# Performance work log

Hardware: AMD Instinct MI355X
Metric: run time of the kernel (lower is better)

## Reference

```python
import jax, jax.numpy as jnp
import numpy as np

# --- static config (matches init_kwargs) ---
DIM_Z, DIM_A, DIM_U, K, GRU_H, DIM_OBS = 32, 16, 4, 8, 64, 16
BATCH, TLEN = 128, 256
Q_STD, R_STD, QR_REG, TEMP = 0.05, 0.05, 1e-3, 1.0


def setup_inputs() -> dict:
    key = jax.random.key(0)
    ks = jax.random.split(key, 10)
    a_seq = jax.random.normal(ks[0], (BATCH, TLEN, DIM_A), jnp.float32)
    h_obs = jax.random.normal(ks[1], (BATCH, DIM_OBS), jnp.float32)
    # scale dynamics so the T-step recursion is stable (spectral radius < 1)
    A_matrices = jax.random.normal(ks[2], (K, DIM_Z, DIM_Z), jnp.float32) * (0.6 / np.sqrt(DIM_Z))
    C_matrices = jax.random.normal(ks[3], (K, DIM_A, DIM_Z), jnp.float32) * (1.0 / np.sqrt(DIM_Z))
    B_matrices = jax.random.normal(ks[4], (K, DIM_Z, DIM_U), jnp.float32) * 0.1
    u_seq = jax.random.normal(ks[5], (BATCH, TLEN, DIM_U), jnp.float32)
    mask = jnp.ones((BATCH, TLEN), jnp.float32)
    # learned params: P_0 = 5*I, cholesky of Q_std*I / R_std*I
    P_0 = 5.0 * jnp.eye(DIM_Z, dtype=jnp.float32)
    mat_Q = np.sqrt(Q_STD).astype(np.float32) * jnp.eye(DIM_Z, dtype=jnp.float32)
    mat_R = np.sqrt(R_STD).astype(np.float32) * jnp.eye(DIM_A, dtype=jnp.float32)
    # alpha network: GRU cell over concat(a_prev, h_obs, z_prev, a_next_all) + linear head
    d_in = DIM_A + DIM_OBS + DIM_Z + K * DIM_A
    gru_Wx = jax.random.normal(ks[6], (d_in, 3 * GRU_H), jnp.float32) / np.sqrt(d_in)
    gru_Wh = jax.random.normal(ks[7], (GRU_H, 3 * GRU_H), jnp.float32) / np.sqrt(GRU_H)
    gru_b = jnp.zeros((3 * GRU_H,), jnp.float32)
    out_W = jax.random.normal(ks[8], (GRU_H, K), jnp.float32) / np.sqrt(GRU_H)
    out_b = jnp.zeros((K,), jnp.float32)
    return dict(a_seq=a_seq, h_obs=h_obs, A_matrices=A_matrices, C_matrices=C_matrices,
                B_matrices=B_matrices, u_seq=u_seq, mask=mask, P_0=P_0, mat_Q=mat_Q,
                mat_R=mat_R, gru_Wx=gru_Wx, gru_Wh=gru_Wh, gru_b=gru_b,
                out_W=out_W, out_b=out_b, epoch=100)


def _mT(M):
    return jnp.swapaxes(M, -1, -2)


def _kf_forward(a_seq, h_obs, A_matrices, C_matrices, B_matrices, u_seq, mask,
                P_0, mat_Q, mat_R, gru_Wx, gru_Wh, gru_b, out_W, out_b):
    Bn, Tn, da = a_seq.shape
    dz = A_matrices.shape[-1]
    I_z = jnp.eye(dz, dtype=a_seq.dtype)
    I_a = jnp.eye(da, dtype=a_seq.dtype)
    Q = mat_Q @ mat_Q.T + QR_REG * I_z
    R = mat_R @ mat_R.T + QR_REG * I_a
    sg = jax.lax.stop_gradient

    def gru_cell(x, h):
        gx = x @ gru_Wx + gru_b
        gh = h @ gru_Wh
        xr, xz, xn = jnp.split(gx, 3, axis=-1)
        hr, hz, hn = jnp.split(gh, 3, axis=-1)
        r = jax.nn.sigmoid(xr + hr)
        zg = jax.nn.sigmoid(xz + hz)
        n = jnp.tanh(xn + r * hn)
        return (1.0 - zg) * n + zg * h

    def step(carry, xs):
        z_prev, P, gh, C_prev = carry
        a_k, u_k, m_k = xs          # [B,da], [B,du], [B]
        mk = m_k[:, None]           # [B,1]
        # per-expert one-step predictions (IMM likelihoods)
        zj = jnp.einsum('kij,bj->bki', A_matrices, z_prev)        # [B,K,dz]
        aj = jnp.einsum('kai,bki->bka', C_matrices, zj)           # [B,K,da]
        a_next_all = aj.reshape(Bn, K * da)
        log_lik = -jnp.sum((a_k[:, None, :] - aj) ** 2, axis=-1)  # [B,K]
        alpha_imm = jax.nn.softmax(log_lik, axis=-1) * mk
        # alpha network (inputs detached as in original)
        a_prev = sg(jnp.einsum('bai,bi->ba', C_prev, z_prev))
        x_in = jnp.concatenate([a_prev, h_obs, sg(z_prev), a_next_all], axis=-1)
        gh = gru_cell(x_in, gh)
        alpha = jax.nn.softmax((gh @ out_W + out_b) / TEMP, axis=-1)  # [B,K]
        # mixture matrices
        A_k = jnp.einsum('bk,kij->bij', alpha, A_matrices)
        C_k = jnp.einsum('bk,kai->bai', alpha, C_matrices)
        # predict / innovate
        z = jnp.einsum('bij,bj->bi', A_k, z_prev)
        a_hat = jnp.einsum('bai,bi->ba', C_k, z)
        r_k = a_k - a_hat
        S = C_k @ P @ _mT(C_k) + R + 1e-4 * I_a
        Kg = _mT(jnp.linalg.solve(_mT(S), C_k @ _mT(P)))          # [B,dz,da]
        Kg = Kg * mk[:, :, None]
        IKC = I_z - Kg @ C_k
        P_f = IKC @ P @ _mT(IKC) + Kg @ R @ _mT(Kg)
        P_f = 0.5 * (P_f + _mT(P_f)) + 1e-3 * I_z
        z_loc = z + jnp.einsum('bia,ba->bi', Kg, r_k)
        tril = jnp.linalg.cholesky(P_f)
        z_filt = z_loc  # eval mode: mean of MVN(z_loc, P_f)
        # epoch >= 20 -> p_true = 0 -> always kalman reconstruction
        a_filt = jnp.einsum('bai,bi->ba', C_k, z_filt)
        z_pred = jnp.einsum('bij,bj->bi', A_k, z_filt)  # eval: no Q-noise
        B_k = jnp.einsum('bk,kiu->biu', alpha, B_matrices)
        z_pred = z_pred + jnp.einsum('biu,bu->bi', B_k, u_k)
        P_p = A_k @ P_f @ _mT(A_k) + Q
        P_p = 0.5 * (P_p + _mT(P_p)) + 1e-3 * I_z
        a_pred = jnp.einsum('bai,bi->ba', C_k, z_pred)
        new_carry = (z_filt, P_p, gh, sg(C_k))
        ys = (z_filt, P_f, z_loc, tril, z_pred, P_p, a_filt, a_pred, S, alpha, alpha_imm)
        return new_carry, ys

    z0 = jnp.zeros((Bn, dz), a_seq.dtype)
    P_init = jnp.broadcast_to(P_0, (Bn, dz, dz))
    gh0 = jnp.zeros((Bn, GRU_H), a_seq.dtype)
    C0 = jnp.broadcast_to(C_matrices[0], (Bn, da, dz))
    xs = (jnp.swapaxes(a_seq, 0, 1), jnp.swapaxes(u_seq, 0, 1), mask.T)
    _, ys = jax.lax.scan(step, (z0, P_init, gh0, C0), xs)
    outs = jax.tree.map(lambda y: jnp.swapaxes(y, 0, 1), ys)  # [T,B,...] -> [B,T,...]
    return outs + (R, Q)


def reference(a_seq, h_obs, A_matrices, C_matrices, B_matrices, u_seq, mask,
              P_0, mat_Q, mat_R, gru_Wx, gru_Wh, gru_b, out_W, out_b, epoch):
    # epoch=100 semantics baked in: temp=1, p_true=0, no burn-in detach, eval mode
    return _kf_forward(a_seq, h_obs, A_matrices, C_matrices, B_matrices, u_seq, mask,
                       P_0, mat_Q, mat_R, gru_Wx, gru_Wh, gru_b, out_W, out_b)
```

## Files before the change

### kernel.cpp

```cpp
#include <hip/hip_runtime.h>
#include <math.h>

#define NT 256
#define FMA4(acc,u,bv) {acc.x+=(u)*(bv).x; acc.y+=(u)*(bv).y; acc.z+=(u)*(bv).z; acc.w+=(u)*(bv).w;}

__device__ __forceinline__ float sigf(float x){ return 1.0f/(1.0f+expf(-x)); }
__device__ __forceinline__ float rdlane(float v, int l){
  return __int_as_float(__builtin_amdgcn_readlane(__float_as_int(v), l));
}
__device__ __forceinline__ float dot4(float4 a, float4 b){
  return a.x*b.x + a.y*b.y + a.z*b.z + a.w*b.w;
}

__launch_bounds__(NT, 1)
__global__ void kf_fwd(const float* __restrict__ a_seq, const float* __restrict__ h_obs,
  const float* __restrict__ Amat, const float* __restrict__ Cmat, const float* __restrict__ Bmat,
  const float* __restrict__ u_seq, const float* __restrict__ mask, const float* __restrict__ P0,
  const float* __restrict__ matQ, const float* __restrict__ matR,
  const float* __restrict__ Wx, const float* __restrict__ Wh, const float* __restrict__ gbias,
  const float* __restrict__ outW, const float* __restrict__ outb, float* __restrict__ out)
{
  constexpr int T=256, B=128;
  constexpr int L6=36, L0=20;
  constexpr size_t BT=(size_t)B*T;
  const size_t off_zf=0;
  const size_t off_Pf=off_zf+BT*32;
  const size_t off_zl=off_Pf+BT*1024;
  const size_t off_tr=off_zl+BT*32;
  const size_t off_zp=off_tr+BT*1024;
  const size_t off_Pp=off_zp+BT*32;
  const size_t off_af=off_Pp+BT*1024;
  const size_t off_ap=off_af+BT*16;
  const size_t off_S =off_ap+BT*16;
  const size_t off_al=off_S +BT*256;
  const size_t off_ai=off_al+BT*8;
  const size_t off_R =off_ai+BT*8;
  const size_t off_Q =off_R +256;

  __shared__ __align__(16) float sA[8*32*L6];
  __shared__ __align__(16) float sC[8*16*L6];
  __shared__ __align__(16) float W12[48*192];
  __shared__ __align__(16) float gxh[192];
  __shared__ __align__(16) float sBm[1024];
  __shared__ __align__(16) float souWT[512];
  __shared__ __align__(16) float soutb8[8];
  __shared__ __align__(16) float P[32*L6], T1m[32*L6], T3m[32*L6], Qm[32*L6];
  __shared__ __align__(16) float Ak2[2][32*L6], AkT2[2][32*L6];
  __shared__ __align__(16) float Ck[16*L6], CPm[16*L6];
  __shared__ __align__(16) float CPT[32*L0], Kg[32*L0];
  __shared__ __align__(16) float Sm[16*L0], Rm[16*L0], Sinv[16*L0];
  __shared__ __align__(16) float Linv[16*17];
  __shared__ __align__(16) float Bk[128];
  __shared__ __align__(16) float zj[256], aj[128];
  __shared__ __align__(16) float gx[192], ghl[192];
  __shared__ __align__(16) float zc[32], znew[32], zloc[32], zpred[32], ghs[64];
  __shared__ __align__(16) float aprevv[16], hob[16];
  __shared__ __align__(16) float ak[16], uk[4], rk[16], alpha8[8];
  __shared__ __align__(16) float ys[16], ws[16];
  __shared__ float mvs2[2];

  const int tid  = threadIdx.x;
  const int wid  = tid>>6;
  const int lane = tid&63;
  const int b = blockIdx.x;

  for (int e=tid; e<8192; e+=NT){ int k=e>>10, i=(e>>5)&31, j=e&31; sA[(k*32+i)*L6+j]=Amat[e]; }
  for (int e=tid; e<4096; e+=NT){ int k=e>>9, a=(e>>5)&15, i=e&31; sC[(k*16+a)*L6+i]=Cmat[e]; }
  for (int e=tid; e<1024; e+=NT) sBm[e]=Bmat[e];
  for (int e=tid; e<512; e+=NT){ int r=e>>6, q=e&63; souWT[r*64+q]=outW[q*8+r]; }
  if (tid<8) soutb8[tid]=outb[tid];
  for (int e=tid; e<1024; e+=NT){
    int i=e>>5, j=e&31;
    float s=0.f;
    #pragma unroll 8
    for (int k=0;k<32;k++) s += matQ[i*32+k]*matQ[j*32+k];
    Qm[i*L6+j]=s+(i==j?0.001f:0.f);
    P[i*L6+j]=P0[e];
  }
  for (int e=tid; e<256; e+=NT){
    int i=e>>4, j=e&15;
    float s=0.f;
    #pragma unroll
    for (int k=0;k<16;k++) s += matR[i*16+k]*matR[j*16+k];
    Rm[i*L0+j]=s+(i==j?0.001f:0.f);
  }
  for (int e=tid; e<16*L6; e+=NT) Ck[e]=0.f;
  if (tid<32) zc[tid]=0.f;
  if (tid<64) ghs[tid]=0.f;
  for (int e=tid; e<192; e+=NT) ghl[e]=0.f;
  if (tid<16) hob[tid]=h_obs[b*16+tid];
  __syncthreads();

  if (tid<48){
    const int c0=tid*4;
    #pragma unroll
    for (int a=0;a<16;a++)
      *(float4*)&W12[(32+a)*192+c0] = *(const float4*)(Wx+(size_t)a*192+c0);
    float4 acc=*(const float4*)(gbias+c0);
    #pragma unroll
    for (int i=0;i<16;i++){
      float4 w=*(const float4*)(Wx+(size_t)(16+i)*192+c0);
      float hv=hob[i];
      FMA4(acc,hv,w);
    }
    *(float4*)&gxh[c0]=acc;
  }
  for (int ic=0; ic<4; ++ic){
    float4 Mi[8];
    if (tid<48){
// ... 30 lines not shown
      #pragma unroll
      for (int ii=0;ii<8;ii++)
        *(float4*)&W12[(ic*8+ii)*192+c0]=Mi[ii];
    }
  }
  if (b==0){
    for (int e=tid;e<256;e+=NT) out[off_R+e]=Rm[(e>>4)*L0+(e&15)];
    for (int e=tid;e<1024;e+=NT) out[off_Q+e]=Qm[(e>>5)*L6+(e&31)];
  }
  __syncthreads();

  for (int t=0;t<T;t++){
    const size_t bt=(size_t)b*T+t;
    const int pc=t&1, pp=pc^1;

    if (wid==0){
      if (lane==0) mvs2[pc]=mask[bt];
      float4 zq[8];
      #pragma unroll
      for (int q=0;q<8;q++) zq[q]=*(const float4*)&zc[q*4];
      if (lane<16){
        float s=0.f;
        #pragma unroll
        for (int q=0;q<8;q++) s+=dot4(*(const float4*)&Ck[lane*L6+q*4], zq[q]);
        aprevv[lane]=s;
      }
      if (lane<48){
        const int c0=lane*4;
        float4 A0=*(const float4*)&gxh[c0];
        float4 A1=make_float4(0.f,0.f,0.f,0.f), A2=A1, A3=A1;
        #pragma unroll
        for (int q=0;q<8;q++){
          float4 zv=zq[q];
          float4 w0=*(const float4*)&W12[(q*4+0)*192+c0];
          float4 w1=*(const float4*)&W12[(q*4+1)*192+c0];
          float4 w2=*(const float4*)&W12[(q*4+2)*192+c0];
          float4 w3=*(const float4*)&W12[(q*4+3)*192+c0];
          FMA4(A0,zv.x,w0); FMA4(A1,zv.y,w1); FMA4(A2,zv.z,w2); FMA4(A3,zv.w,w3);
        }
        #pragma unroll
        for (int q=0;q<4;q++){
          float4 av=*(const float4*)&aprevv[q*4];
          float4 w0=*(const float4*)&W12[(32+q*4+0)*192+c0];
          float4 w1=*(const float4*)&W12[(32+q*4+1)*192+c0];
          float4 w2=*(const float4*)&W12[(32+q*4+2)*192+c0];
          float4 w3=*(const float4*)&W12[(32+q*4+3)*192+c0];
          FMA4(A0,av.x,w0); FMA4(A1,av.y,w1); FMA4(A2,av.z,w2); FMA4(A3,av.w,w3);
// ... 5 lines not shown
      {
        float r =sigf(gx[lane]+ghl[lane]);
        float zg=sigf(gx[64+lane]+ghl[64+lane]);
        float n =tanhf(gx[128+lane]+r*ghl[128+lane]);
        float h=ghs[lane];
        ghs[lane]=(1.f-zg)*n+zg*h;
      }
      if (lane<8){
        float s=soutb8[lane];
        #pragma unroll
        for (int q=0;q<16;q++){
          float4 g=*(const float4*)&ghs[q*4];
          float4 w=*(const float4*)&souWT[lane*64+q*4];
          s+=dot4(g,w);
        }
        float m8=s;
        m8=fmaxf(m8,__shfl_xor(m8,1)); m8=fmaxf(m8,__shfl_xor(m8,2)); m8=fmaxf(m8,__shfl_xor(m8,4));
        float e2=expf(s-m8);
        float ss=e2;
        ss+=__shfl_xor(ss,1); ss+=__shfl_xor(ss,2); ss+=__shfl_xor(ss,4);
        float av=e2/ss;
        alpha8[lane]=av;
        out[off_al+bt*8+lane]=av;
      }
    } else if (wid==1){
      if (t>0){
        const size_t bt1=bt-1;
        #pragma unroll
        for (int q=0;q<4;q++){
          int e=lane+64*q; int a2=e>>4, b2=e&15;
          float s=0.f;
          #pragma unroll
          for (int k=0;k<16;k++) s+=Linv[k*17+a2]*Linv[k*17+b2];
          Sinv[a2*L0+b2]=s;
        }
        {
          int i0=lane>>2, aq=lane&3;
          float4 k0=make_float4(0.f,0.f,0.f,0.f), k1=k0;
          #pragma unroll
          for (int q=0;q<4;q++){
            float4 ca=*(const float4*)&CPT[i0*L0+q*4];
            float4 cb=*(const float4*)&CPT[(i0+16)*L0+q*4];
            float4 v0=*(const float4*)&Sinv[(q*4+0)*L0+aq*4];
            float4 v1=*(const float4*)&Sinv[(q*4+1)*L0+aq*4];
            float4 v2=*(const float4*)&Sinv[(q*4+2)*L0+aq*4];
            float4 v3=*(const float4*)&Sinv[(q*4+3)*L0+aq*4];
// ... 25 lines not shown
            FMA4(q0,-a0.y,bv); FMA4(q1,-a1.y,bv); FMA4(q2,-a2.y,bv); FMA4(q3,-a3.y,bv);
            bv=*(const float4*)&CPm[(q*4+2)*L6+j0];
            FMA4(q0,-a0.z,bv); FMA4(q1,-a1.z,bv); FMA4(q2,-a2.z,bv); FMA4(q3,-a3.z,bv);
            bv=*(const float4*)&CPm[(q*4+3)*L6+j0];
            FMA4(q0,-a0.w,bv); FMA4(q1,-a1.w,bv); FMA4(q2,-a2.w,bv); FMA4(q3,-a3.w,bv);
          }
          int d0=i0-j0;
          if (d0>=0&&d0<4){ if(d0==0)q0.x+=1e-3f; else if(d0==1)q0.y+=1e-3f; else if(d0==2)q0.z+=1e-3f; else q0.w+=1e-3f; }
          int d1=i0+1-j0;
          if (d1>=0&&d1<4){ if(d1==0)q1.x+=1e-3f; else if(d1==1)q1.y+=1e-3f; else if(d1==2)q1.z+=1e-3f; else q1.w+=1e-3f; }
          int d2=i0+2-j0;
          if (d2>=0&&d2<4){ if(d2==0)q2.x+=1e-3f; else if(d2==1)q2.y+=1e-3f; else if(d2==2)q2.z+=1e-3f; else q2.w+=1e-3f; }
          int d3=i0+3-j0;
          if (d3>=0&&d3<4){ if(d3==0)q3.x+=1e-3f; else if(d3==1)q3.y+=1e-3f; else if(d3==2)q3.z+=1e-3f; else q3.w+=1e-3f; }
          *(float4*)&T3m[(i0+0)*L6+j0]=q0;
          *(float4*)&T3m[(i0+1)*L6+j0]=q1;
          *(float4*)&T3m[(i0+2)*L6+j0]=q2;
          *(float4*)&T3m[(i0+3)*L6+j0]=q3;
          *(float4*)&out[off_Pf+bt1*1024+(i0+0)*32+j0]=q0;
          *(float4*)&out[off_Pf+bt1*1024+(i0+1)*32+j0]=q1;
          *(float4*)&out[off_Pf+bt1*1024+(i0+2)*32+j0]=q2;
          *(float4*)&out[off_Pf+bt1*1024+(i0+3)*32+j0]=q3;
        }
      }
    } else if (wid==2){
      if (t>0){
        const size_t bt1=bt-1;
        float4 zq[8];
        #pragma unroll
        for (int q=0;q<8;q++) zq[q]=*(const float4*)&zc[q*4];
        if (lane<32){
          float s=0.f;
          #pragma unroll
          for (int q=0;q<8;q++) s+=dot4(*(const float4*)&Ak2[pp][lane*L6+q*4], zq[q]);
          float4 bk=*(const float4*)&Bk[lane*4];
          float4 u4=*(const float4*)&uk[0];
          s+=dot4(bk,u4);
          zpred[lane]=s;
          out[off_zp+bt1*32+lane]=s;
        }
        if (lane>=32 && lane<48){
          int a=lane-32;
          float s=0.f;
          #pragma unroll
          for (int q=0;q<8;q++) s+=dot4(*(const float4*)&Ck[a*L6+q*4], zq[q]);
          out[off_af+bt1*16+a]=s;
        }
        if (lane<16){
          float s=0.f;
          #pragma unroll
          for (int q=0;q<8;q++)
            s+=dot4(*(const float4*)&Ck[lane*L6+q*4], *(const float4*)&zpred[q*4]);
          out[off_ap+bt1*16+lane]=s;
        }
      }
    } else {
      if (lane<16) ak[lane]=a_seq[bt*16+lane];
      float mv=mask[bt];
      float4 zq[8];
      #pragma unroll
      for (int q=0;q<8;q++) zq[q]=*(const float4*)&zc[q*4];
      #pragma unroll
      for (int r=0;r<4;r++){
        int e=lane+64*r; int k=e>>5, i=e&31;
        float s=0.f;
        #pragma unroll
        for (int q=0;q<8;q++) s+=dot4(*(const float4*)&sA[(k*32+i)*L6+q*4], zq[q]);
        zj[e]=s;
      }
      #pragma unroll
      for (int r=0;r<2;r++){
        int e=lane+64*r; int k=e>>4, a=e&15;
        float s=0.f;
        #pragma unroll
        for (int q=0;q<8;q++) s+=dot4(*(const float4*)&sC[(k*16+a)*L6+q*4], *(const float4*)&zj[k*32+q*4]);
        aj[e]=s;
      }
      if (lane<8){
        float s=0.f;
        #pragma unroll
        for (int q=0;q<4;q++){
          float4 av=*(const float4*)&ak[q*4];
          float4 jv=*(const float4*)&aj[lane*16+q*4];
          float dx=av.x-jv.x, dy=av.y-jv.y, dz=av.z-jv.z, dw=av.w-jv.w;
          s+=dx*dx+dy*dy+dz*dz+dw*dw;
        }
        float llv=-s;
        float m8=llv;
        m8=fmaxf(m8,__shfl_xor(m8,1)); m8=fmaxf(m8,__shfl_xor(m8,2)); m8=fmaxf(m8,__shfl_xor(m8,4));
        float e2=expf(llv-m8);
        float ss=e2;
        ss+=__shfl_xor(ss,1); ss+=__shfl_xor(ss,2); ss+=__shfl_xor(ss,4);
        out[off_ai+bt*8+lane]=e2/ss*mv;
      }
    }
    __syncthreads();

    if (wid==0 || wid==3){
      float alr[8];
      float4 a0v=*(const float4*)&alpha8[0], a1v=*(const float4*)&alpha8[4];
      alr[0]=a0v.x; alr[1]=a0v.y; alr[2]=a0v.z; alr[3]=a0v.w;
      alr[4]=a1v.x; alr[5]=a1v.y; alr[6]=a1v.z; alr[7]=a1v.w;
      if (wid==0){
        #pragma unroll
        for (int r=0;r<2;r++){
          int e=lane+64*r; int i=e>>3, qd=e&7;
          float4 acc=make_float4(0.f,0.f,0.f,0.f);
          #pragma unroll
          for (int k=0;k<8;k++){
            float4 av=*(const float4*)&sA[(k*32+i)*L6+qd*4];
            FMA4(acc,alr[k],av);
          }
          *(float4*)&Ak2[pc][i*L6+qd*4]=acc;
          AkT2[pc][(qd*4+0)*L6+i]=acc.x; AkT2[pc][(qd*4+1)*L6+i]=acc.y;
          AkT2[pc][(qd*4+2)*L6+i]=acc.z; AkT2[pc][(qd*4+3)*L6+i]=acc.w;
        }
        #pragma unroll
        for (int r=0;r<2;r++){
          int e=lane+64*r;
          float s=0.f;
          #pragma unroll
          for (int k=0;k<8;k++) s+=alr[k]*sBm[k*128+e];
          Bk[e]=s;
        }
        if (lane<32){
          float s=0.f;
          #pragma unroll
          for (int k=0;k<8;k++) s+=alr[k]*zj[k*32+lane];
          znew[lane]=s;
        }
      } else {
        #pragma unroll
        for (int r=2;r<4;r++){
          int e=lane+64*r; int i=e>>3, qd=e&7;
          float4 acc=make_float4(0.f,0.f,0.f,0.f);
          #pragma unroll
          for (int k=0;k<8;k++){
            float4 av=*(const float4*)&sA[(k*32+i)*L6+qd*4];
            FMA4(acc,alr[k],av);
          }
          *(float4*)&Ak2[pc][i*L6+qd*4]=acc;
          AkT2[pc][(qd*4+0)*L6+i]=acc.x; AkT2[pc][(qd*4+1)*L6+i]=acc.y;
          AkT2[pc][(qd*4+2)*L6+i]=acc.z; AkT2[pc][(qd*4+3)*L6+i]=acc.w;
        }
        #pragma unroll
        for (int r=0;r<2;r++){
          int e=lane+64*r; int a=e>>3, qd=e&7;
          float4 acc=make_float4(0.f,0.f,0.f,0.f);
          #pragma unroll
          for (int k=0;k<8;k++){
            float4 cv=*(const float4*)&sC[(k*16+a)*L6+qd*4];
            FMA4(acc,alr[k],cv);
          }
          *(float4*)&Ck[a*L6+qd*4]=acc;
        }
      }
    } else if (wid==1){
      if (t>0){
        const size_t bt1=bt-1;
        int row=lane<32?lane:31;
        float trl[32];
        #pragma unroll
        for (int q=0;q<8;q++){
          float4 v=*(const float4*)&T3m[row*L6+q*4];
          trl[q*4+0]=v.x; trl[q*4+1]=v.y; trl[q*4+2]=v.z; trl[q*4+3]=v.w;
        }
        #pragma unroll
        for (int c=0;c<32;c++){
          float d=rdlane(trl[c],c);
          float inv=rsqrtf(d);
          float lc=(lane==c)?d*inv:trl[c]*inv;
          trl[c]=lc;
          #pragma unroll
          for (int j=c+1;j<32;j++) trl[j]-=lc*rdlane(lc,j);
        }
        if (lane<32){
          #pragma unroll
          for (int q=0;q<8;q++){
            float t0=(q*4+0<=lane)?trl[q*4+0]:0.f;
            float t1=(q*4+1<=lane)?trl[q*4+1]:0.f;
            float t2=(q*4+2<=lane)?trl[q*4+2]:0.f;
            float t3=(q*4+3<=lane)?trl[q*4+3]:0.f;
            *(float4*)&out[off_tr+bt1*1024+lane*32+q*4]=make_float4(t0,t1,t2,t3);
          }
        }
      }
    } else {
      if (t>0){
        const size_t bt1=bt-1;
        {
          const int i0=(lane>>3)*4, j0=(lane&7)*4;
          float4 q0=make_float4(0.f,0.f,0.f,0.f), q1=q0, q2=q0, q3=q0;
          #pragma unroll 4
          for (int q=0;q<8;q++){
            float4 a0=*(const float4*)&Ak2[pp][(i0+0)*L6+q*4];
            float4 a1=*(const float4*)&Ak2[pp][(i0+1)*L6+q*4];
            float4 a2=*(const float4*)&Ak2[pp][(i0+2)*L6+q*4];
            float4 a3=*(const float4*)&Ak2[pp][(i0+3)*L6+q*4];
            float4 bv;
            bv=*(const float4*)&T3m[(q*4+0)*L6+j0];
            FMA4(q0,a0.x,bv); FMA4(q1,a1.x,bv); FMA4(q2,a2.x,bv); FMA4(q3,a3.x,bv);
            bv=*(const float4*)&T3m[(q*4+1)*L6+j0];
            FMA4(q0,a0.y,bv); FMA4(q1,a1.y,bv); FMA4(q2,a2.y,bv); FMA4(q3,a3.y,bv);
            bv=*(const float4*)&T3m[(q*4+2)*L6+j0];
            FMA4(q0,a0.z,bv); FMA4(q1,a1.z,bv); FMA4(q2,a2.z,bv); FMA4(q3,a3.z,bv);
            bv=*(const float4*)&T3m[(q*4+3)*L6+j0];
            FMA4(q0,a0.w,bv); FMA4(q1,a1.w,bv); FMA4(q2,a2.w,bv); FMA4(q3,a3.w,bv);
          }
          *(float4*)&T1m[(i0+0)*L6+j0]=q0;
          *(float4*)&T1m[(i0+1)*L6+j0]=q1;
          *(float4*)&T1m[(i0+2)*L6+j0]=q2;
          *(float4*)&T1m[(i0+3)*L6+j0]=q3;
// ... 18 lines not shown
            float4 a1=*(const float4*)&T1m[(i0+1)*L6+q*4];
            float4 a2=*(const float4*)&T1m[(i0+2)*L6+q*4];
            float4 a3=*(const float4*)&T1m[(i0+3)*L6+q*4];
            float4 bv;
            bv=*(const float4*)&AkT2[pp][(q*4+0)*L6+j0];
            FMA4(q0,a0.x,bv); FMA4(q1,a1.x,bv); FMA4(q2,a2.x,bv); FMA4(q3,a3.x,bv);
            bv=*(const float4*)&AkT2[pp][(q*4+1)*L6+j0];
            FMA4(q0,a0.y,bv); FMA4(q1,a1.y,bv); FMA4(q2,a2.y,bv); FMA4(q3,a3.y,bv);
            bv=*(const float4*)&AkT2[pp][(q*4+2)*L6+j0];
            FMA4(q0,a0.z,bv); FMA4(q1,a1.z,bv); FMA4(q2,a2.z,bv); FMA4(q3,a3.z,bv);
            bv=*(const float4*)&AkT2[pp][(q*4+3)*L6+j0];
            FMA4(q0,a0.w,bv); FMA4(q1,a1.w,bv); FMA4(q2,a2.w,bv); FMA4(q3,a3.w,bv);
          }
          *(float4*)&P[(i0+0)*L6+j0]=q0;
          *(float4*)&P[(i0+1)*L6+j0]=q1;
          *(float4*)&P[(i0+2)*L6+j0]=q2;
          *(float4*)&P[(i0+3)*L6+j0]=q3;
          *(float4*)&out[off_Pp+bt1*1024+(i0+0)*32+j0]=q0;
          *(float4*)&out[off_Pp+bt1*1024+(i0+1)*32+j0]=q1;
          *(float4*)&out[off_Pp+bt1*1024+(i0+2)*32+j0]=q2;
          *(float4*)&out[off_Pp+bt1*1024+(i0+3)*32+j0]=q3;
        }
      }
    }
    __syncthreads();

    if (wid==0){
      {
        int qd=lane&7, a0=lane>>3;
        float4 d0=make_float4(0.f,0.f,0.f,0.f), d1=d0;
        #pragma unroll 2
        for (int q=0;q<8;q++){
          float4 c0=*(const float4*)&Ck[a0*L6+q*4];
          float4 c1=*(const float4*)&Ck[(a0+8)*L6+q*4];
          float4 p0=*(const float4*)&P[(q*4+0)*L6+qd*4];
          float4 p1=*(const float4*)&P[(q*4+1)*L6+qd*4];
          float4 p2=*(const float4*)&P[(q*4+2)*L6+qd*4];
          float4 p3=*(const float4*)&P[(q*4+3)*L6+qd*4];
          FMA4(d0,c0.x,p0); FMA4(d0,c0.y,p1); FMA4(d0,c0.z,p2); FMA4(d0,c0.w,p3);
          FMA4(d1,c1.x,p0); FMA4(d1,c1.y,p1); FMA4(d1,c1.z,p2); FMA4(d1,c1.w,p3);
        }
        *(float4*)&CPm[a0*L6+qd*4]=d0;
        *(float4*)&CPm[(a0+8)*L6+qd*4]=d1;
        CPT[(qd*4+0)*L0+a0]=d0.x; CPT[(qd*4+1)*L0+a0]=d0.y;
        CPT[(qd*4+2)*L0+a0]=d0.z; CPT[(qd*4+3)*L0+a0]=d0.w;
        CPT[(qd*4+0)*L0+a0+8]=d1.x; CPT[(qd*4+1)*L0+a0+8]=d1.y;
        CPT[(qd*4+2)*L0+a0+8]=d1.z; CPT[(qd*4+3)*L0+a0+8]=d1.w;
      }
      if (lane<16){
        float s=0.f;
        #pragma unroll
        for (int q=0;q<8;q++) s+=dot4(*(const float4*)&Ck[lane*L6+q*4], *(const float4*)&znew[q*4]);
        rk[lane]=ak[lane]-s;
      }
      {
        int a2=lane>>2, cq=lane&3;
        float s0=0.f,s1=0.f,s2=0.f,s3=0.f;
        #pragma unroll 2
        for (int q=0;q<8;q++){
          float4 cp=*(const float4*)&CPm[a2*L6+q*4];
          s0+=dot4(cp,*(const float4*)&Ck[(cq*4+0)*L6+q*4]);
          s1+=dot4(cp,*(const float4*)&Ck[(cq*4+1)*L6+q*4]);
          s2+=dot4(cp,*(const float4*)&Ck[(cq*4+2)*L6+q*4]);
          s3+=dot4(cp,*(const float4*)&Ck[(cq*4+3)*L6+q*4]);
        }
        float4 rm=*(const float4*)&Rm[a2*L0+cq*4];
        s0+=rm.x+((a2==cq*4+0)?1e-4f:0.f);
        s1+=rm.y+((a2==cq*4+1)?1e-4f:0.f);
        s2+=rm.z+((a2==cq*4+2)?1e-4f:0.f);
        s3+=rm.w+((a2==cq*4+3)?1e-4f:0.f);
        float4 sv=make_float4(s0,s1,s2,s3);
        *(float4*)&Sm[a2*L0+cq*4]=sv;
        *(float4*)&out[off_S+bt*256+lane*4]=sv;
      }
      {
        int row=lane<16?lane:15;
        float Sr[16], invd[16];
        #pragma unroll
        for (int q=0;q<4;q++){
          float4 v=*(const float4*)&Sm[row*L0+q*4];
          Sr[q*4+0]=v.x; Sr[q*4+1]=v.y; Sr[q*4+2]=v.z; Sr[q*4+3]=v.w;
        }
        #pragma unroll
        for (int c=0;c<16;c++){
          float d=rdlane(Sr[c],c);
          float inv=rsqrtf(d);
          invd[c]=inv;
// ... 37 lines not shown
          s+=dot4(*(const float4*)&CPT[lane*L0+q*4], *(const float4*)&ws[q*4]);
        zloc[lane]=s;
        zc[lane]=s;
        out[off_zf+bt*32+lane]=s;
        out[off_zl+bt*32+lane]=s;
      }
    } else if (wid==1){
      if (lane<48){
        const int c0=lane*4;
        float4 A0=make_float4(0.f,0.f,0.f,0.f), A1=A0, A2=A0, A3=A0;
        #pragma unroll
        for (int q=0;q<16;q++){
          float4 gv=*(const float4*)&ghs[q*4];
          float4 w0=*(const float4*)(Wh+(size_t)(q*4+0)*192+c0);
          float4 w1=*(const float4*)(Wh+(size_t)(q*4+1)*192+c0);
          float4 w2=*(const float4*)(Wh+(size_t)(q*4+2)*192+c0);
          float4 w3=*(const float4*)(Wh+(size_t)(q*4+3)*192+c0);
          FMA4(A0,gv.x,w0); FMA4(A1,gv.y,w1); FMA4(A2,gv.z,w2); FMA4(A3,gv.w,w3);
        }
        float4 g=make_float4(A0.x+A1.x+A2.x+A3.x, A0.y+A1.y+A2.y+A3.y,
                             A0.z+A1.z+A2.z+A3.z, A0.w+A1.w+A2.w+A3.w);
        *(float4*)&ghl[c0]=g;
      }
    } else if (wid==2){
      if (lane<4) uk[lane]=u_seq[bt*4+lane];
    }
    __syncthreads();
  }

  {
    const size_t btL=(size_t)b*T+(T-1);
    const int pl=(T-1)&1;
    if (wid==1){
      #pragma unroll
      for (int q=0;q<4;q++){
        int e=lane+64*q; int a2=e>>4, b2=e&15;
        float s=0.f;
        #pragma unroll
        for (int k=0;k<16;k++) s+=Linv[k*17+a2]*Linv[k*17+b2];
        Sinv[a2*L0+b2]=s;
      }
      {
        int i0=lane>>2, aq=lane&3;
        float4 k0=make_float4(0.f,0.f,0.f,0.f), k1=k0;
        #pragma unroll
        for (int q=0;q<4;q++){
          float4 ca=*(const float4*)&CPT[i0*L0+q*4];
          float4 cb=*(const float4*)&CPT[(i0+16)*L0+q*4];
// ... 29 lines not shown
          FMA4(q0,-a0.y,bv); FMA4(q1,-a1.y,bv); FMA4(q2,-a2.y,bv); FMA4(q3,-a3.y,bv);
          bv=*(const float4*)&CPm[(q*4+2)*L6+j0];
          FMA4(q0,-a0.z,bv); FMA4(q1,-a1.z,bv); FMA4(q2,-a2.z,bv); FMA4(q3,-a3.z,bv);
          bv=*(const float4*)&CPm[(q*4+3)*L6+j0];
          FMA4(q0,-a0.w,bv); FMA4(q1,-a1.w,bv); FMA4(q2,-a2.w,bv); FMA4(q3,-a3.w,bv);
        }
        int d0=i0-j0;
        if (d0>=0&&d0<4){ if(d0==0)q0.x+=1e-3f; else if(d0==1)q0.y+=1e-3f; else if(d0==2)q0.z+=1e-3f; else q0.w+=1e-3f; }
        int d1=i0+1-j0;
        if (d1>=0&&d1<4){ if(d1==0)q1.x+=1e-3f; else if(d1==1)q1.y+=1e-3f; else if(d1==2)q1.z+=1e-3f; else q1.w+=1e-3f; }
        int d2=i0+2-j0;
        if (d2>=0&&d2<4){ if(d2==0)q2.x+=1e-3f; else if(d2==1)q2.y+=1e-3f; else if(d2==2)q2.z+=1e-3f; else q2.w+=1e-3f; }
        int d3=i0+3-j0;
        if (d3>=0&&d3<4){ if(d3==0)q3.x+=1e-3f; else if(d3==1)q3.y+=1e-3f; else if(d3==2)q3.z+=1e-3f; else q3.w+=1e-3f; }
        *(float4*)&T3m[(i0+0)*L6+j0]=q0;
        *(float4*)&T3m[(i0+1)*L6+j0]=q1;
        *(float4*)&T3m[(i0+2)*L6+j0]=q2;
        *(float4*)&T3m[(i0+3)*L6+j0]=q3;
        *(float4*)&out[off_Pf+btL*1024+(i0+0)*32+j0]=q0;
        *(float4*)&out[off_Pf+btL*1024+(i0+1)*32+j0]=q1;
        *(float4*)&out[off_Pf+btL*1024+(i0+2)*32+j0]=q2;
        *(float4*)&out[off_Pf+btL*1024+(i0+3)*32+j0]=q3;
      }
    } else if (wid==2){
      float4 zq[8];
      #pragma unroll
      for (int q=0;q<8;q++) zq[q]=*(const float4*)&zc[q*4];
      if (lane<32){
        float s=0.f;
        #pragma unroll
        for (int q=0;q<8;q++) s+=dot4(*(const float4*)&Ak2[pl][lane*L6+q*4], zq[q]);
        float4 bk=*(const float4*)&Bk[lane*4];
        float4 u4=*(const float4*)&uk[0];
        s+=dot4(bk,u4);
        zpred[lane]=s;
        out[off_zp+btL*32+lane]=s;
      }
      if (lane>=32 && lane<48){
        int a=lane-32;
        float s=0.f;
        #pragma unroll
        for (int q=0;q<8;q++) s+=dot4(*(const float4*)&Ck[a*L6+q*4], zq[q]);
        out[off_af+btL*16+a]=s;
      }
      if (lane<16){
        float s=0.f;
        #pragma unroll
        for (int q=0;q<8;q++)
          s+=dot4(*(const float4*)&Ck[lane*L6+q*4], *(const float4*)&zpred[q*4]);
        out[off_ap+btL*16+lane]=s;
      }
    }
    __syncthreads();
    if (wid==1){
      int row=lane<32?lane:31;
      float trl[32];
      #pragma unroll
      for (int q=0;q<8;q++){
        float4 v=*(const float4*)&T3m[row*L6+q*4];
        trl[q*4+0]=v.x; trl[q*4+1]=v.y; trl[q*4+2]=v.z; trl[q*4+3]=v.w;
      }
      #pragma unroll
      for (int c=0;c<32;c++){
        float d=rdlane(trl[c],c);
        float inv=rsqrtf(d);
        float lc=(lane==c)?d*inv:trl[c]*inv;
        trl[c]=lc;
        #pragma unroll
        for (int j=c+1;j<32;j++) trl[j]-=lc*rdlane(lc,j);
      }
      if (lane<32){
        #pragma unroll
        for (int q=0;q<8;q++){
          float t0=(q*4+0<=lane)?trl[q*4+0]:0.f;
          float t1=(q*4+1<=lane)?trl[q*4+1]:0.f;
          float t2=(q*4+2<=lane)?trl[q*4+2]:0.f;
          float t3=(q*4+3<=lane)?trl[q*4+3]:0.f;
          *(float4*)&out[off_tr+btL*1024+lane*32+q*4]=make_float4(t0,t1,t2,t3);
        }
      }
    } else if (wid==2){
      {
        const int i0=(lane>>3)*4, j0=(lane&7)*4;
        float4 q0=make_float4(0.f,0.f,0.f,0.f), q1=q0, q2=q0, q3=q0;
        #pragma unroll 4
        for (int q=0;q<8;q++){
          float4 a0=*(const float4*)&Ak2[pl][(i0+0)*L6+q*4];
          float4 a1=*(const float4*)&Ak2[pl][(i0+1)*L6+q*4];
          float4 a2=*(const float4*)&Ak2[pl][(i0+2)*L6+q*4];
          float4 a3=*(const float4*)&Ak2[pl][(i0+3)*L6+q*4];
          float4 bv;
          bv=*(const float4*)&T3m[(q*4+0)*L6+j0];
          FMA4(q0,a0.x,bv); FMA4(q1,a1.x,bv); FMA4(q2,a2.x,bv); FMA4(q3,a3.x,bv);
          bv=*(const float4*)&T3m[(q*4+1)*L6+j0];
          FMA4(q0,a0.y,bv); FMA4(q1,a1.y,bv); FMA4(q2,a2.y,bv); FMA4(q3,a3.y,bv);
          bv=*(const float4*)&T3m[(q*4+2)*L6+j0];
          FMA4(q0,a0.z,bv); FMA4(q1,a1.z,bv); FMA4(q2,a2.z,bv); FMA4(q3,a3.z,bv);
          bv=*(const float4*)&T3m[(q*4+3)*L6+j0];
          FMA4(q0,a0.w,bv); FMA4(q1,a1.w,bv); FMA4(q2,a2.w,bv); FMA4(q3,a3.w,bv);
        }
        *(float4*)&T1m[(i0+0)*L6+j0]=q0;
        *(float4*)&T1m[(i0+1)*L6+j0]=q1;
        *(float4*)&T1m[(i0+2)*L6+j0]=q2;
        *(float4*)&T1m[(i0+3)*L6+j0]=q3;
// ... 13 lines not shown
        int d3=i0+3-j0;
        if (d3>=0&&d3<4){ if(d3==0)q3.x+=1e-3f; else if(d3==1)q3.y+=1e-3f; else if(d3==2)q3.z+=1e-3f; else q3.w+=1e-3f; }
        #pragma unroll 4
        for (int q=0;q<8;q++){
          float4 a0=*(const float4*)&T1m[(i0+0)*L6+q*4];
          float4 a1=*(const float4*)&T1m[(i0+1)*L6+q*4];
          float4 a2=*(const float4*)&T1m[(i0+2)*L6+q*4];
          float4 a3=*(const float4*)&T1m[(i0+3)*L6+q*4];
          float4 bv;
          bv=*(const float4*)&AkT2[pl][(q*4+0)*L6+j0];
          FMA4(q0,a0.x,bv); FMA4(q1,a1.x,bv); FMA4(q2,a2.x,bv); FMA4(q3,a3.x,bv);
          bv=*(const float4*)&AkT2[pl][(q*4+1)*L6+j0];
          FMA4(q0,a0.y,bv); FMA4(q1,a1.y,bv); FMA4(q2,a2.y,bv); FMA4(q3,a3.y,bv);
          bv=*(const float4*)&AkT2[pl][(q*4+2)*L6+j0];
          FMA4(q0,a0.z,bv); FMA4(q1,a1.z,bv); FMA4(q2,a2.z,bv); FMA4(q3,a3.z,bv);
          bv=*(const float4*)&AkT2[pl][(q*4+3)*L6+j0];
          FMA4(q0,a0.w,bv); FMA4(q1,a1.w,bv); FMA4(q2,a2.w,bv); FMA4(q3,a3.w,bv);
        }
        *(float4*)&out[off_Pp+btL*1024+(i0+0)*32+j0]=q0;
        *(float4*)&out[off_Pp+btL*1024+(i0+1)*32+j0]=q1;
        *(float4*)&out[off_Pp+btL*1024+(i0+2)*32+j0]=q2;
        *(float4*)&out[off_Pp+btL*1024+(i0+3)*32+j0]=q3;
      }
    }
  }
}

extern "C" void kernel_launch(void* const* d_in, const int* in_sizes, int n_in,
                              void* d_out, int out_size, void* d_ws, size_t ws_size,
                              hipStream_t stream) {
  kf_fwd<<<128, NT, 0, stream>>>(
    (const float*)d_in[0],
    (const float*)d_in[1],
    (const float*)d_in[2],
    (const float*)d_in[3],
    (const float*)d_in[4],
    (const float*)d_in[5],
    (const float*)d_in[6],
    (const float*)d_in[7],
    (const float*)d_in[8],
    (const float*)d_in[9],
    (const float*)d_in[10],
    (const float*)d_in[11],
    (const float*)d_in[12],
    (const float*)d_in[13],
    (const float*)d_in[14],
// ... 3 lines not shown
```

Baseline: 2.626 ms.

## Reschedule per-step warp work to remove a barrier phase per timestep

Warp 0 now builds the mixed C matrix immediately after the softmax, into a double-buffered Ck2. Each step's work is redistributed across the four warps: the Cholesky factorisation moves to warp 2, the mixed A/B construction moves to warp 3, and the P-prediction matmul moves to warp 1. The intent is to drop one of the three __syncthreads phases per timestep and balance the critical path across warps. In exchange, the extra C buffer adds shared memory, and the warp handling the Cholesky and A mixing now carries a heavier serial load.

Measured after the change: 2.407 ms, median of 2. 1.09x faster.

```diff
diff --git a/kernel.cpp b/kernel.cpp
--- a/kernel.cpp
+++ b/kernel.cpp
@@ -46,7 +46,8 @@
   __shared__ __align__(16) float soutb8[8];
   __shared__ __align__(16) float P[32*L6], T1m[32*L6], T3m[32*L6], Qm[32*L6];
   __shared__ __align__(16) float Ak2[2][32*L6], AkT2[2][32*L6];
-  __shared__ __align__(16) float Ck[16*L6], CPm[16*L6];
+  __shared__ __align__(16) float Ck2[2][16*L6];
+  __shared__ __align__(16) float CPm[16*L6];
   __shared__ __align__(16) float CPT[32*L0], Kg[32*L0];
   __shared__ __align__(16) float Sm[16*L0], Rm[16*L0], Sinv[16*L0];
   __shared__ __align__(16) float Linv[16*17];
@@ -84,7 +85,7 @@
     for (int k=0;k<16;k++) s += matR[i*16+k]*matR[j*16+k];
     Rm[i*L0+j]=s+(i==j?0.001f:0.f);
   }
-  for (int e=tid; e<16*L6; e+=NT) Ck[e]=0.f;
+  for (int e=tid; e<16*L6; e+=NT){ Ck2[0][e]=0.f; Ck2[1][e]=0.f; }
   if (tid<32) zc[tid]=0.f;
   if (tid<64) ghs[tid]=0.f;
   for (int e=tid; e<192; e+=NT) ghl[e]=0.f;
@@ -161,7 +162,7 @@
       if (lane<16){
         float s=0.f;
         #pragma unroll
-        for (int q=0;q<8;q++) s+=dot4(*(const float4*)&Ck[lane*L6+q*4], zq[q]);
+        for (int q=0;q<8;q++) s+=dot4(*(const float4*)&Ck2[pp][lane*L6+q*4], zq[q]);
         aprevv[lane]=s;
       }
       if (lane<48){
@@ -213,6 +214,23 @@
         float av=e2/ss;
         alpha8[lane]=av;
         out[off_al+bt*8+lane]=av;
+      }
+      {
+        float alr[8];
+        float4 a0v=*(const float4*)&alpha8[0], a1v=*(const float4*)&alpha8[4];
+        alr[0]=a0v.x; alr[1]=a0v.y; alr[2]=a0v.z; alr[3]=a0v.w;
+        alr[4]=a1v.x; alr[5]=a1v.y; alr[6]=a1v.z; alr[7]=a1v.w;
+        #pragma unroll
+        for (int r=0;r<2;r++){
+          int e=lane+64*r; int a=e>>3, qd=e&7;
+          float4 acc=make_float4(0.f,0.f,0.f,0.f);
+          #pragma unroll
+          for (int k=0;k<8;k++){
+            float4 cv=*(const float4*)&sC[(k*16+a)*L6+qd*4];
+            FMA4(acc,alr[k],cv);
+          }
+          *(float4*)&Ck2[pc][a*L6+qd*4]=acc;
+        }
       }
     } else if (wid==1){
       if (t>0){
@@ -284,172 +302,6 @@
           *(float4*)&out[off_Pf+bt1*1024+(i0+2)*32+j0]=q2;
           *(float4*)&out[off_Pf+bt1*1024+(i0+3)*32+j0]=q3;
         }
-      }
-    } else if (wid==2){
-      if (t>0){
-        const size_t bt1=bt-1;
-        float4 zq[8];
-        #pragma unroll
-        for (int q=0;q<8;q++) zq[q]=*(const float4*)&zc[q*4];
-        if (lane<32){
-          float s=0.f;
-          #pragma unroll
-          for (int q=0;q<8;q++) s+=dot4(*(const float4*)&Ak2[pp][lane*L6+q*4], zq[q]);
-          float4 bk=*(const float4*)&Bk[lane*4];
-          float4 u4=*(const float4*)&uk[0];
-          s+=dot4(bk,u4);
-          zpred[lane]=s;
-          out[off_zp+bt1*32+lane]=s;
-        }
-        if (lane>=32 && lane<48){
-          int a=lane-32;
-          float s=0.f;
-          #pragma unroll
-          for (int q=0;q<8;q++) s+=dot4(*(const float4*)&Ck[a*L6+q*4], zq[q]);
-          out[off_af+bt1*16+a]=s;
-        }
-        if (lane<16){
-          float s=0.f;
-          #pragma unroll
-          for (int q=0;q<8;q++)
-            s+=dot4(*(const float4*)&Ck[lane*L6+q*4], *(const float4*)&zpred[q*4]);
-          out[off_ap+bt1*16+lane]=s;
-        }
-      }
-    } else {
-      if (lane<16) ak[lane]=a_seq[bt*16+lane];
-      float mv=mask[bt];
-      float4 zq[8];
-      #pragma unroll
-      for (int q=0;q<8;q++) zq[q]=*(const float4*)&zc[q*4];
-      #pragma unroll
-      for (int r=0;r<4;r++){
-        int e=lane+64*r; int k=e>>5, i=e&31;
-        float s=0.f;
-        #pragma unroll
-        for (int q=0;q<8;q++) s+=dot4(*(const float4*)&sA[(k*32+i)*L6+q*4], zq[q]);
-        zj[e]=s;
-      }
-      #pragma unroll
-      for (int r=0;r<2;r++){
-        int e=lane+64*r; int k=e>>4, a=e&15;
-        float s=0.f;
-        #pragma unroll
-        for (int q=0;q<8;q++) s+=dot4(*(const float4*)&sC[(k*16+a)*L6+q*4], *(const float4*)&zj[k*32+q*4]);
-        aj[e]=s;
-      }
-      if (lane<8){
-        float s=0.f;
-        #pragma unroll
-        for (int q=0;q<4;q++){
-          float4 av=*(const float4*)&ak[q*4];
-          float4 jv=*(const float4*)&aj[lane*16+q*4];
-          float dx=av.x-jv.x, dy=av.y-jv.y, dz=av.z-jv.z, dw=av.w-jv.w;
-          s+=dx*dx+dy*dy+dz*dz+dw*dw;
-        }
-        float llv=-s;
-        float m8=llv;
-        m8=fmaxf(m8,__shfl_xor(m8,1)); m8=fmaxf(m8,__shfl_xor(m8,2)); m8=fmaxf(m8,__shfl_xor(m8,4));
-        float e2=expf(llv-m8);
-        float ss=e2;
-        ss+=__shfl_xor(ss,1); ss+=__shfl_xor(ss,2); ss+=__shfl_xor(ss,4);
-        out[off_ai+bt*8+lane]=e2/ss*mv;
-      }
-    }
-    __syncthreads();
-
-    if (wid==0 || wid==3){
-      float alr[8];
-      float4 a0v=*(const float4*)&alpha8[0], a1v=*(const float4*)&alpha8[4];
-      alr[0]=a0v.x; alr[1]=a0v.y; alr[2]=a0v.z; alr[3]=a0v.w;
-      alr[4]=a1v.x; alr[5]=a1v.y; alr[6]=a1v.z; alr[7]=a1v.w;
-      if (wid==0){
-        #pragma unroll
-        for (int r=0;r<2;r++){
-          int e=lane+64*r; int i=e>>3, qd=e&7;
-          float4 acc=make_float4(0.f,0.f,0.f,0.f);
-          #pragma unroll
-          for (int k=0;k<8;k++){
-            float4 av=*(const float4*)&sA[(k*32+i)*L6+qd*4];
-            FMA4(acc,alr[k],av);
-          }
-          *(float4*)&Ak2[pc][i*L6+qd*4]=acc;
-          AkT2[pc][(qd*4+0)*L6+i]=acc.x; AkT2[pc][(qd*4+1)*L6+i]=acc.y;
-          AkT2[pc][(qd*4+2)*L6+i]=acc.z; AkT2[pc][(qd*4+3)*L6+i]=acc.w;
-        }
-        #pragma unroll
-        for (int r=0;r<2;r++){
-          int e=lane+64*r;
-          float s=0.f;
-          #pragma unroll
-          for (int k=0;k<8;k++) s+=alr[k]*sBm[k*128+e];
-          Bk[e]=s;
-        }
-        if (lane<32){
-          float s=0.f;
-          #pragma unroll
-          for (int k=0;k<8;k++) s+=alr[k]*zj[k*32+lane];
-          znew[lane]=s;
-        }
-      } else {
-        #pragma unroll
-        for (int r=2;r<4;r++){
-          int e=lane+64*r; int i=e>>3, qd=e&7;
-          float4 acc=make_float4(0.f,0.f,0.f,0.f);
-          #pragma unroll
-          for (int k=0;k<8;k++){
-            float4 av=*(const float4*)&sA[(k*32+i)*L6+qd*4];
-            FMA4(acc,alr[k],av);
-          }
-          *(float4*)&Ak2[pc][i*L6+qd*4]=acc;
-          AkT2[pc][(qd*4+0)*L6+i]=acc.x; AkT2[pc][(qd*4+1)*L6+i]=acc.y;
-          AkT2[pc][(qd*4+2)*L6+i]=acc.z; AkT2[pc][(qd*4+3)*L6+i]=acc.w;
-        }
-        #pragma unroll
-        for (int r=0;r<2;r++){
-          int e=lane+64*r; int a=e>>3, qd=e&7;
-          float4 acc=make_float4(0.f,0.f,0.f,0.f);
-          #pragma unroll
-          for (int k=0;k<8;k++){
-            float4 cv=*(const float4*)&sC[(k*16+a)*L6+qd*4];
-            FMA4(acc,alr[k],cv);
-          }
-          *(float4*)&Ck[a*L6+qd*4]=acc;
-        }
-      }
-    } else if (wid==1){
-      if (t>0){
-        const size_t bt1=bt-1;
-        int row=lane<32?lane:31;
-        float trl[32];
-        #pragma unroll
-        for (int q=0;q<8;q++){
-          float4 v=*(const float4*)&T3m[row*L6+q*4];
-          trl[q*4+0]=v.x; trl[q*4+1]=v.y; trl[q*4+2]=v.z; trl[q*4+3]=v.w;
-        }
-        #pragma unroll
-        for (int c=0;c<32;c++){
-          float d=rdlane(trl[c],c);
-          float inv=rsqrtf(d);
-          float lc=(lane==c)?d*inv:trl[c]*inv;
-          trl[c]=lc;
-          #pragma unroll
-          for (int j=c+1;j<32;j++) trl[j]-=lc*rdlane(lc,j);
-        }
-        if (lane<32){
-          #pragma unroll
-          for (int q=0;q<8;q++){
-            float t0=(q*4+0<=lane)?trl[q*4+0]:0.f;
-            float t1=(q*4+1<=lane)?trl[q*4+1]:0.f;
-            float t2=(q*4+2<=lane)?trl[q*4+2]:0.f;
-            float t3=(q*4+3<=lane)?trl[q*4+3]:0.f;
-            *(float4*)&out[off_tr+bt1*1024+lane*32+q*4]=make_float4(t0,t1,t2,t3);
-          }
-        }
-      }
-    } else {
-      if (t>0){
-        const size_t bt1=bt-1;
         {
           const int i0=(lane>>3)*4, j0=(lane&7)*4;
           float4 q0=make_float4(0.f,0.f,0.f,0.f), q1=q0, q2=q0, q3=q0;
@@ -514,17 +366,93 @@
           *(float4*)&out[off_Pp+bt1*1024+(i0+3)*32+j0]=q3;
         }
       }
+    } else if (wid==2){
+      if (t>0){
+        const size_t bt1=bt-1;
+        float4 zq[8];
+        #pragma unroll
+        for (int q=0;q<8;q++) zq[q]=*(const float4*)&zc[q*4];
+        if (lane<32){
+          float s=0.f;
+          #pragma unroll
+          for (int q=0;q<8;q++) s+=dot4(*(const float4*)&Ak2[pp][lane*L6+q*4], zq[q]);
+          float4 bk=*(const float4*)&Bk[lane*4];
+          float4 u4=*(const float4*)&uk[0];
+          s+=dot4(bk,u4);
+          zpred[lane]=s;
+          out[off_zp+bt1*32+lane]=s;
+        }
+        if (lane>=32 && lane<48){
+          int a=lane-32;
+          float s=0.f;
+          #pragma unroll
+          for (int q=0;q<8;q++) s+=dot4(*(const float4*)&Ck2[pp][a*L6+q*4], zq[q]);
+          out[off_af+bt1*16+a]=s;
+        }
+        if (lane<16){
+          float s=0.f;
+          #pragma unroll
+          for (int q=0;q<8;q++)
+            s+=dot4(*(const float4*)&Ck2[pp][lane*L6+q*4], *(const float4*)&zpred[q*4]);
+          out[off_ap+bt1*16+lane]=s;
+        }
+      }
+    } else {
+      if (lane<16) ak[lane]=a_seq[bt*16+lane];
+      float mv=mask[bt];
+      float4 zq[8];
+      #pragma unroll
+      for (int q=0;q<8;q++) zq[q]=*(const float4*)&zc[q*4];
+      #pragma unroll
+      for (int r=0;r<4;r++){
+        int e=lane+64*r; int k=e>>5, i=e&31;
+        float s=0.f;
+        #pragma unroll
+        for (int q=0;q<8;q++) s+=dot4(*(const float4*)&sA[(k*32+i)*L6+q*4], zq[q]);
+        zj[e]=s;
+      }
+      #pragma unroll
+      for (int r=0;r<2;r++){
+        int e=lane+64*r; int k=e>>4, a=e&15;
+        float s=0.f;
+        #pragma unroll
+        for (int q=0;q<8;q++) s+=dot4(*(const float4*)&sC[(k*16+a)*L6+q*4], *(const float4*)&zj[k*32+q*4]);
+        aj[e]=s;
+      }
+      if (lane<8){
+        float s=0.f;
+        #pragma unroll
+        for (int q=0;q<4;q++){
+          float4 av=*(const float4*)&ak[q*4];
+          float4 jv=*(const float4*)&aj[lane*16+q*4];
+          float dx=av.x-jv.x, dy=av.y-jv.y, dz=av.z-jv.z, dw=av.w-jv.w;
+          s+=dx*dx+dy*dy+dz*dz+dw*dw;
+        }
+        float llv=-s;
+        float m8=llv;
+        m8=fmaxf(m8,__shfl_xor(m8,1)); m8=fmaxf(m8,__shfl_xor(m8,2)); m8=fmaxf(m8,__shfl_xor(m8,4));
+        float e2=expf(llv-m8);
+        float ss=e2;
+        ss+=__shfl_xor(ss,1); ss+=__shfl_xor(ss,2); ss+=__shfl_xor(ss,4);
+        out[off_ai+bt*8+lane]=e2/ss*mv;
+      }
     }
     __syncthreads();
 
     if (wid==0){
+      if (lane<32){
+        float4 a0v=*(const float4*)&alpha8[0], a1v=*(const float4*)&alpha8[4];
+        float s=a0v.x*zj[lane]+a0v.y*zj[32+lane]+a0v.z*zj[64+lane]+a0v.w*zj[96+lane]
+               +a1v.x*zj[128+lane]+a1v.y*zj[160+lane]+a1v.z*zj[192+lane]+a1v.w*zj[224+lane];
+        znew[lane]=s;
+      }
       {
         int qd=lane&7, a0=lane>>3;
         float4 d0=make_float4(0.f,0.f,0.f,0.f), d1=d0;
         #pragma unroll 2
         for (int q=0;q<8;q++){
-          float4 c0=*(const float4*)&Ck[a0*L6+q*4];
-          float4 c1=*(const float4*)&Ck[(a0+8)*L6+q*4];
+          float4 c0=*(const float4*)&Ck2[pc][a0*L6+q*4];
+          float4 c1=*(const float4*)&Ck2[pc][(a0+8)*L6+q*4];
           float4 p0=*(const float4*)&P[(q*4+0)*L6+qd*4];
           float4 p1=*(const float4*)&P[(q*4+1)*L6+qd*4];
           float4 p2=*(const float4*)&P[(q*4+2)*L6+qd*4];
@@ -542,7 +470,7 @@
       if (lane<16){
         float s=0.f;
         #pragma unroll
-        for (int q=0;q<8;q++) s+=dot4(*(const float4*)&Ck[lane*L6+q*4], *(const float4*)&znew[q*4]);
+        for (int q=0;q<8;q++) s+=dot4(*(const float4*)&Ck2[pc][lane*L6+q*4], *(const float4*)&znew[q*4]);
         rk[lane]=ak[lane]-s;
       }
       {
@@ -551,10 +479,10 @@
         #pragma unroll 2
         for (int q=0;q<8;q++){
           float4 cp=*(const float4*)&CPm[a2*L6+q*4];
-          s0+=dot4(cp,*(const float4*)&Ck[(cq*4+0)*L6+q*4]);
-          s1+=dot4(cp,*(const float4*)&Ck[(cq*4+1)*L6+q*4]);
-          s2+=dot4(cp,*(const float4*)&Ck[(cq*4+2)*L6+q*4]);
-          s3+=dot4(cp,*(const float4*)&Ck[(cq*4+3)*L6+q*4]);
+          s0+=dot4(cp,*(const float4*)&Ck2[pc][(cq*4+0)*L6+q*4]);
+          s1+=dot4(cp,*(const float4*)&Ck2[pc][(cq*4+1)*L6+q*4]);
+          s2+=dot4(cp,*(const float4*)&Ck2[pc][(cq*4+2)*L6+q*4]);
+          s3+=dot4(cp,*(const float4*)&Ck2[pc][(cq*4+3)*L6+q*4]);
         }
         float4 rm=*(const float4*)&Rm[a2*L0+cq*4];
         s0+=rm.x+((a2==cq*4+0)?1e-4f:0.f);
@@ -638,8 +566,63 @@
                              A0.z+A1.z+A2.z+A3.z, A0.w+A1.w+A2.w+A3.w);
         *(float4*)&ghl[c0]=g;
       }
+      if (lane>=48 && lane<52) uk[lane-48]=u_seq[bt*4+(lane-48)];
     } else if (wid==2){
-      if (lane<4) uk[lane]=u_seq[bt*4+lane];
+      if (t>0){
+        const size_t bt1=bt-1;
+        int row=lane<32?lane:31;
+        float trl[32];
+        #pragma unroll
+        for (int q=0;q<8;q++){
+          float4 v=*(const float4*)&T3m[row*L6+q*4];
+          trl[q*4+0]=v.x; trl[q*4+1]=v.y; trl[q*4+2]=v.z; trl[q*4+3]=v.w;
+        }
+        #pragma unroll
+        for (int c=0;c<32;c++){
+          float d=rdlane(trl[c],c);
+          float inv=rsqrtf(d);
+          float lc=(lane==c)?d*inv:trl[c]*inv;
+          trl[c]=lc;
+          #pragma unroll
+          for (int j=c+1;j<32;j++) trl[j]-=lc*rdlane(lc,j);
+        }
+        if (lane<32){
+          #pragma unroll
+          for (int q=0;q<8;q++){
+            float t0=(q*4+0<=lane)?trl[q*4+0]:0.f;
+            float t1=(q*4+1<=lane)?trl[q*4+1]:0.f;
+            float t2=(q*4+2<=lane)?trl[q*4+2]:0.f;
+            float t3=(q*4+3<=lane)?trl[q*4+3]:0.f;
+            *(float4*)&out[off_tr+bt1*1024+lane*32+q*4]=make_float4(t0,t1,t2,t3);
+          }
+        }
+      }
+    } else {
+      float alr[8];
+      float4 a0v=*(const float4*)&alpha8[0], a1v=*(const float4*)&alpha8[4];
+      alr[0]=a0v.x; alr[1]=a0v.y; alr[2]=a0v.z; alr[3]=a0v.w;
+      alr[4]=a1v.x; alr[5]=a1v.y; alr[6]=a1v.z; alr[7]=a1v.w;
+      #pragma unroll
+      for (int r=0;r<4;r++){
+        int e=lane+64*r; int i=e>>3, qd=e&7;
+        float4 acc=make_float4(0.f,0.f,0.f,0.f);
+        #pragma unroll
+        for (int k=0;k<8;k++){
+          float4 av=*(const float4*)&sA[(k*32+i)*L6+qd*4];
+          FMA4(acc,alr[k],av);
+        }
+        *(float4*)&Ak2[pc][i*L6+qd*4]=acc;
+        AkT2[pc][(qd*4+0)*L6+i]=acc.x; AkT2[pc][(qd*4+1)*L6+i]=acc.y;
+        AkT2[pc][(qd*4+2)*L6+i]=acc.z; AkT2[pc][(qd*4+3)*L6+i]=acc.w;
+      }
+      #pragma unroll
+      for (int r=0;r<2;r++){
+        int e=lane+64*r;
+        float s=0.f;
+        #pragma unroll
+        for (int k=0;k<8;k++) s+=alr[k]*sBm[k*128+e];
+        Bk[e]=s;
+      }
     }
     __syncthreads();
   }
@@ -715,64 +698,6 @@
         *(float4*)&out[off_Pf+btL*1024+(i0+2)*32+j0]=q2;
         *(float4*)&out[off_Pf+btL*1024+(i0+3)*32+j0]=q3;
       }
-    } else if (wid==2){
-      float4 zq[8];
-      #pragma unroll
-      for (int q=0;q<8;q++) zq[q]=*(const float4*)&zc[q*4];
-      if (lane<32){
-        float s=0.f;
-        #pragma unroll
-        for (int q=0;q<8;q++) s+=dot4(*(const float4*)&Ak2[pl][lane*L6+q*4], zq[q]);
-        float4 bk=*(const float4*)&Bk[lane*4];
-        float4 u4=*(const float4*)&uk[0];
-        s+=dot4(bk,u4);
-        zpred[lane]=s;
-        out[off_zp+btL*32+lane]=s;
-      }
-      if (lane>=32 && lane<48){
-        int a=lane-32;
-        float s=0.f;
-        #pragma unroll
-        for (int q=0;q<8;q++) s+=dot4(*(const float4*)&Ck[a*L6+q*4], zq[q]);
-        out[off_af+btL*16+a]=s;
-      }
-      if (lane<16){
-        float s=0.f;
-        #pragma unroll
-        for (int q=0;q<8;q++)
-          s+=dot4(*(const float4*)&Ck[lane*L6+q*4], *(const float4*)&zpred[q*4]);
-        out[off_ap+btL*16+lane]=s;
-      }
-    }
-    __syncthreads();
-    if (wid==1){
-      int row=lane<32?lane:31;
-      float trl[32];
-      #pragma unroll
-      for (int q=0;q<8;q++){
-        float4 v=*(const float4*)&T3m[row*L6+q*4];
-        trl[q*4+0]=v.x; trl[q*4+1]=v.y; trl[q*4+2]=v.z; trl[q*4+3]=v.w;
-      }
-      #pragma unroll
-      for (int c=0;c<32;c++){
-        float d=rdlane(trl[c],c);
-        float inv=rsqrtf(d);
-        float lc=(lane==c)?d*inv:trl[c]*inv;
-        trl[c]=lc;
-        #pragma unroll
-        for (int j=c+1;j<32;j++) trl[j]-=lc*rdlane(lc,j);
-      }
-      if (lane<32){
-        #pragma unroll
-        for (int q=0;q<8;q++){
-          float t0=(q*4+0<=lane)?trl[q*4+0]:0.f;
-          float t1=(q*4+1<=lane)?trl[q*4+1]:0.f;
-          float t2=(q*4+2<=lane)?trl[q*4+2]:0.f;
-          float t3=(q*4+3<=lane)?trl[q*4+3]:0.f;
-          *(float4*)&out[off_tr+btL*1024+lane*32+q*4]=make_float4(t0,t1,t2,t3);
-        }
-      }
-    } else if (wid==2){
       {
         const int i0=(lane>>3)*4, j0=(lane&7)*4;
         float4 q0=make_float4(0.f,0.f,0.f,0.f), q1=q0, q2=q0, q3=q0;
@@ -832,6 +757,63 @@
         *(float4*)&out[off_Pp+btL*1024+(i0+2)*32+j0]=q2;
         *(float4*)&out[off_Pp+btL*1024+(i0+3)*32+j0]=q3;
       }
+    } else if (wid==2){
+      float4 zq[8];
+      #pragma unroll
+      for (int q=0;q<8;q++) zq[q]=*(const float4*)&zc[q*4];
+      if (lane<32){
+        float s=0.f;
+        #pragma unroll
+        for (int q=0;q<8;q++) s+=dot4(*(const float4*)&Ak2[pl][lane*L6+q*4], zq[q]);
+        float4 bk=*(const float4*)&Bk[lane*4];
+        float4 u4=*(const float4*)&uk[0];
+        s+=dot4(bk,u4);
+        zpred[lane]=s;
+        out[off_zp+btL*32+lane]=s;
+      }
+      if (lane>=32 && lane<48){
+        int a=lane-32;
+        float s=0.f;
+        #pragma unroll
+        for (int q=0;q<8;q++) s+=dot4(*(const float4*)&Ck2[pl][a*L6+q*4], zq[q]);
+        out[off_af+btL*16+a]=s;
+      }
+      if (lane<16){
+        float s=0.f;
+        #pragma unroll
+        for (int q=0;q<8;q++)
+          s+=dot4(*(const float4*)&Ck2[pl][lane*L6+q*4], *(const float4*)&zpred[q*4]);
+        out[off_ap+btL*16+lane]=s;
+      }
+    }
+    __syncthreads();
+    if (wid==2){
+      int row=lane<32?lane:31;
+      float trl[32];
+      #pragma unroll
+      for (int q=0;q<8;q++){
+        float4 v=*(const float4*)&T3m[row*L6+q*4];
+        trl[q*4+0]=v.x; trl[q*4+1]=v.y; trl[q*4+2]=v.z; trl[q*4+3]=v.w;
+      }
+      #pragma unroll
+      for (int c=0;c<32;c++){
+        float d=rdlane(trl[c],c);
+        float inv=rsqrtf(d);
+        float lc=(lane==c)?d*inv:trl[c]*inv;
+        trl[c]=lc;
+        #pragma unroll
+        for (int j=c+1;j<32;j++) trl[j]-=lc*rdlane(lc,j);
+      }
+      if (lane<32){
+        #pragma unroll
+        for (int q=0;q<8;q++){
+          float t0=(q*4+0<=lane)?trl[q*4+0]:0.f;
+          float t1=(q*4+1<=lane)?trl[q*4+1]:0.f;
+          float t2=(q*4+2<=lane)?trl[q*4+2]:0.f;
+          float t3=(q*4+3<=lane)?trl[q*4+3]:0.f;
+          *(float4*)&out[off_tr+btL*1024+lane*32+q*4]=make_float4(t0,t1,t2,t3);
+        }
+      }
     }
   }
 }
```
